# Kernel optimization log

Hardware: AMD Instinct MI355X
Metric: run time of the kernel (lower is better)

## Reference

```python
import jax, jax.numpy as jnp
import numpy as np

B, S, H = 1, 1024, 1024
E = 1024          # expert_dim
NEXP = 16         # num_experts
TOPK = 2
ALPHA = 1.702
LIMIT = 7.0


def setup_inputs() -> dict:
    key = jax.random.key(0)
    ks = jax.random.split(key, 8)
    hidden_states = jax.random.normal(ks[0], (B, S, H), dtype=jnp.float32)
    # router (gate): Linear(H, NEXP) with bias
    Wg = jax.random.normal(ks[1], (NEXP, H), dtype=jnp.float32) / np.sqrt(H)
    bg = jax.random.normal(ks[2], (NEXP,), dtype=jnp.float32) * 0.01
    # per-expert gate_up_proj: Linear(H, 2E) -> store as [NEXP, H, 2E]
    Wgu = jax.random.normal(ks[3], (NEXP, H, 2 * E), dtype=jnp.float32) / np.sqrt(H)
    bgu = jax.random.normal(ks[4], (NEXP, 2 * E), dtype=jnp.float32) * 0.01
    # per-expert down_proj: Linear(E, H) -> store as [NEXP, E, H]
    Wd = jax.random.normal(ks[5], (NEXP, E, H), dtype=jnp.float32) / np.sqrt(E)
    bd = jax.random.normal(ks[6], (NEXP, H), dtype=jnp.float32) * 0.01
    return {"hidden_states": hidden_states, "Wg": Wg, "bg": bg,
            "Wgu": Wgu, "bgu": bgu, "Wd": Wd, "bd": bd}


def _moe_forward(x, Wg, bg, Wgu, bgu, Wd, bd):
    b, s, h = x.shape
    xt = x.reshape(-1, h)                                   # [T, H]
    # router
    logits = xt @ Wg.T + bg                                 # [T, NEXP]
    # gpt_oss routing: topk over raw logits, softmax over selected
    top_vals, top_idx = jax.lax.top_k(logits, TOPK)         # [T, K]
    rw = jax.nn.softmax(top_vals.astype(jnp.float32), axis=-1).astype(xt.dtype)
    # combine weight per (token, expert): zero for unselected experts
    onehot = jax.nn.one_hot(top_idx, NEXP, dtype=xt.dtype)  # [T, K, NEXP]
    cw = jnp.einsum("tk,tke->te", rw, onehot)               # [T, NEXP]
    # dense expert compute (reference math identical to gather/scatter version)
    gu = jnp.einsum("th,ehf->tef", xt, Wgu) + bgu[None]     # [T, NEXP, 2E]
    gate = gu[..., ::2]
    up = gu[..., 1::2]
    gate = jnp.minimum(gate, LIMIT)
    up = jnp.clip(up, -LIMIT, LIMIT)
    glu = gate * jax.nn.sigmoid(gate * ALPHA)
    gated = (up + 1.0) * glu                                # [T, NEXP, E]
    out_e = jnp.einsum("tef,efh->teh", gated, Wd) + bd[None]  # [T, NEXP, H]
    out = jnp.einsum("teh,te->th", out_e, cw)               # [T, H]
    return out.reshape(b, s, h)


def reference(hidden_states, Wg, bg, Wgu, bgu, Wd, bd):
    return _moe_forward(hidden_states, Wg, bg, Wgu, bgu, Wd, bd)
```

## Files before the change

kernel.cpp:

```cpp
#include <hip/hip_runtime.h>
#include <hip/hip_bf16.h>

#define NT 1024
#define HD 1024
#define ED 1024
#define F2D 2048
#define NEXPERT 16
#define GROWS 2304
#define ALPHA_C 1.702f
#define LIMIT_C 7.0f

typedef float f32x4 __attribute__((ext_vector_type(4)));
typedef float fv4 __attribute__((ext_vector_type(4)));
typedef short short8 __attribute__((ext_vector_type(8)));
typedef unsigned int u32x4 __attribute__((ext_vector_type(4)));

__device__ __forceinline__ unsigned short f2bf(float x) {
  union { float f; unsigned int u; } v; v.f = x;
  unsigned int r = v.u + 0x7FFFu + ((v.u >> 16) & 1u);
  return (unsigned short)(r >> 16);
}
__device__ __forceinline__ unsigned int pk2(float lo, float hi) {
  return (unsigned int)f2bf(lo) | ((unsigned int)f2bf(hi) << 16);
}
__device__ __forceinline__ fv4 ldnt4(const float* p) {
  return __builtin_nontemporal_load((const fv4*)p);
}
__device__ __forceinline__ void async16(const void* g, void* l) {
  __builtin_amdgcn_global_load_lds((const __attribute__((address_space(1))) void*)g,
                                   (__attribute__((address_space(3))) void*)l, 16, 0, 0);
}

__global__ __launch_bounds__(64) void k_router(const float* __restrict__ x,
                                               const float* __restrict__ Wg,
                                               const float* __restrict__ bg,
                                               const float* __restrict__ bd,
                                               int* __restrict__ e01,
                                               float* __restrict__ w0f,
                                               float* __restrict__ w1f,
                                               unsigned short* __restrict__ Xbf,
                                               float* __restrict__ out) {
  const int t = blockIdx.x;
  const int l = threadIdx.x;
  const float4* x4 = (const float4*)(x + (size_t)t * HD);
  for (int i = 0; i < 4; ++i) {
    const int idx = l + 64 * i;
    float4 v = x4[idx];
    unsigned int a = pk2(v.x, v.y);
    unsigned int b = pk2(v.z, v.w);
    unsigned int* dst = (unsigned int*)(Xbf + (size_t)t * HD + idx * 4);
    dst[0] = a; dst[1] = b;
  }
  const int e = l & 15, qq = l >> 4;
  const float4* wg4 = (const float4*)(Wg + (size_t)e * HD);
  float s0a = 0.f, s1a = 0.f;
#pragma unroll 8
  for (int j = 0; j < 32; ++j) {
    const int i0 = qq + 8 * j;
    const int i1 = i0 + 4;
    float4 a0 = x4[i0], b0 = wg4[i0];
    float4 a1 = x4[i1], b1 = wg4[i1];
    s0a += a0.x * b0.x + a0.y * b0.y + a0.z * b0.z + a0.w * b0.w;
    s1a += a1.x * b1.x + a1.y * b1.y + a1.z * b1.z + a1.w * b1.w;
  }
  float s = s0a + s1a;
  s += __shfl_xor(s, 16);
  s += __shfl_xor(s, 32);
  const float logit = s + bg[e];
  float v0 = -1e30f, v1 = -1e30f; int i0 = 0, i1 = 0;
  for (int k = 0; k < 16; ++k) {
    float lv = __shfl(logit, k);
    if (lv > v0) { v1 = v0; i1 = i0; v0 = lv; i0 = k; }
    else if (lv > v1) { v1 = lv; i1 = k; }
  }
  const float w0 = 1.f / (1.f + __expf(v1 - v0));
  const float w1 = 1.f - w0;
  if (l == 0) {
    e01[t] = i0 | (i1 << 8);
    w0f[t] = w0;
    w1f[t] = w1;
  }
  const float4* bd0 = (const float4*)(bd + (size_t)i0 * HD);
  const float4* bd1 = (const float4*)(bd + (size_t)i1 * HD);
  float4* o4 = (float4*)(out + (size_t)t * HD);
  for (int i = 0; i < 4; ++i) {
    const int idx = l + 64 * i;
    float4 a = bd0[idx], b = bd1[idx];
    float4 r;
    r.x = w0 * a.x + w1 * b.x;
    r.y = w0 * a.y + w1 * b.y;
    r.z = w0 * a.z + w1 * b.z;
    r.w = w0 * a.w + w1 * b.w;
    o4[idx] = r;
  }
}

__global__ __launch_bounds__(1024) void k_scan(const int* __restrict__ e01,
                                               const float* __restrict__ w0f,
                                               const float* __restrict__ w1f,
                                               int* __restrict__ cnt,
                                               int* __restrict__ off,
                                               int* __restrict__ gtok,
                                               float* __restrict__ gwt) {
  __shared__ int scnt[NEXPERT];
  __shared__ int soff[NEXPERT];
  __shared__ int scur[NEXPERT];
  const int t = threadIdx.x;
  if (t < NEXPERT) { scnt[t] = 0; scur[t] = 0; }
  __syncthreads();
  const int p = e01[t];
  const int e0 = p & 255, e1 = p >> 8;
  atomicAdd(&scnt[e0], 1);
  atomicAdd(&scnt[e1], 1);
  __syncthreads();
  if (t == 0) {
    int a = 0;
    for (int e = 0; e < NEXPERT; ++e) { soff[e] = a; off[e] = a; cnt[e] = scnt[e]; a += scnt[e]; }
  }
  __syncthreads();
  int s0 = atomicAdd(&scur[e0], 1);
  gtok[soff[e0] + s0] = t; gwt[soff[e0] + s0] = w0f[t];
  int s1 = atomicAdd(&scur[e1], 1);
  gtok[soff[e1] + s1] = t; gwt[soff[e1] + s1] = w1f[t];
}

#define BSTG1 132
__global__ __launch_bounds__(512, 1) void k_gemm1(const unsigned short* __restrict__ Xbf,
                                                  const float* __restrict__ Wgu,
                                                  const float* __restrict__ bgu,
                                                  const int* __restrict__ cnt,
                                                  const int* __restrict__ off,
                                                  const int* __restrict__ gtok,
                                                  unsigned short* __restrict__ Gact) {
  const int e = blockIdx.z;
  const int Ne = cnt[e];
  const int mtile = blockIdx.y;
  if (mtile * 256 >= Ne) return;
  const int ntile = blockIdx.x;
  const int tid = threadIdx.x;
  const int lane = tid & 63;
  const int wv = tid >> 6;
  const int wm = wv >> 1;
  const int wn = wv & 1;
  const int q = lane >> 4;
  const int fr = lane & 15;
  const int base = off[e] + mtile * 256;

  __shared__ unsigned short Alds[2][256 * 32];
  __shared__ unsigned int Blds[2][16 * BSTG1];

  const int ar0 = wv * 32 + (lane >> 2);
  const int ar1 = ar0 + 16;
  const int ags0 = base + (((mtile * 256 + ar0) < Ne) ? ar0 : 0);
  const int ags1 = base + (((mtile * 256 + ar1) < Ne) ? ar1 : 0);
  const unsigned short* agp0 = Xbf + (size_t)gtok[ags0] * HD + (lane & 3) * 8;
  const unsigned short* agp1 = Xbf + (size_t)gtok[ags1] * HD + (lane & 3) * 8;
  const int aofs = wv * 1024;

  const int p2 = tid >> 5;
  const int bc = tid & 31;
  const float* Wb = Wgu + (size_t)e * HD * F2D + (size_t)(2 * p2) * F2D + ntile * 128 + bc * 4;

  f32x4 acc[4][4] = {};
  fv4 b0, b1;

  b0 = ldnt4(Wb);
  b1 = ldnt4(Wb + F2D);
  async16(agp0, Alds[0] + aofs);
  async16(agp1, Alds[0] + aofs + 512);
  {
    u32x4 pkv;
    pkv[0] = pk2(b0[0], b1[0]); pkv[1] = pk2(b0[1], b1[1]);
    pkv[2] = pk2(b0[2], b1[2]); pkv[3] = pk2(b0[3], b1[3]);
    *(u32x4*)(Blds[0] + p2 * BSTG1 + bc * 4) = pkv;
  }
  __syncthreads();

  for (int ks = 0; ks < 32; ++ks) {
    const int cur = ks & 1, nxt = cur ^ 1;
    const bool more = (ks + 1) < 32;
    if (more) {
      const float* bp = Wb + (size_t)(ks + 1) * 32 * F2D;
      b0 = ldnt4(bp);
      b1 = ldnt4(bp + F2D);
      async16(agp0 + (ks + 1) * 32, Alds[nxt] + aofs);
      async16(agp1 + (ks + 1) * 32, Alds[nxt] + aofs + 512);
    }
    short8 af[4], bfr[4];
#pragma unroll
    for (int mi = 0; mi < 4; ++mi)
      af[mi] = *(const short8*)(Alds[cur] + (wm * 64 + mi * 16 + fr) * 32 + q * 8);
#pragma unroll
    for (int ni = 0; ni < 4; ++ni) {
      const unsigned int* p = Blds[cur] + (q * 4) * BSTG1 + wn * 64 + ni * 16 + fr;
      union { unsigned int u[4]; short8 s; } uu;
      uu.u[0] = p[0]; uu.u[1] = p[BSTG1]; uu.u[2] = p[2 * BSTG1]; uu.u[3] = p[3 * BSTG1];
      bfr[ni] = uu.s;
    }
#pragma unroll
    for (int mi = 0; mi < 4; ++mi)
#pragma unroll
      for (int ni = 0; ni < 4; ++ni)
        acc[mi][ni] = __builtin_amdgcn_mfma_f32_16x16x32_bf16(af[mi], bfr[ni], acc[mi][ni], 0, 0, 0);
    if (more) {
      u32x4 pkv;
      pkv[0] = pk2(b0[0], b1[0]); pkv[1] = pk2(b0[1], b1[1]);
      pkv[2] = pk2(b0[2], b1[2]); pkv[3] = pk2(b0[3], b1[3]);
      *(u32x4*)(Blds[nxt] + p2 * BSTG1 + bc * 4) = pkv;
    }
    __syncthreads();
  }

  const float* bguE = bgu + (size_t)e * F2D + ntile * 128;
#pragma unroll
  for (int mi = 0; mi < 4; ++mi) {
#pragma unroll
    for (int ni = 0; ni < 4; ++ni) {
      const int coll = wn * 64 + ni * 16 + fr;
      const float bias = bguE[coll];
#pragma unroll
      for (int r = 0; r < 4; ++r) {
        const int srow = wm * 64 + mi * 16 + q * 4 + r;
        float v = acc[mi][ni][r] + bias;
        float pv = __shfl_xor(v, 1);
        float gate = (lane & 1) ? pv : v;
        float up   = (lane & 1) ? v : pv;
        gate = fminf(gate, LIMIT_C);
        up = fminf(fmaxf(up, -LIMIT_C), LIMIT_C);
        float glu = gate / (1.f + __expf(-ALPHA_C * gate));
        float val = (up + 1.f) * glu;
        if (!(lane & 1) && (mtile * 256 + srow) < Ne)
          Gact[(size_t)(base + srow) * ED + ((ntile * 128 + coll) >> 1)] = f2bf(val);
      }
    }
  }
}

#define BSTG2 68
__global__ __launch_bounds__(512, 2) void k_gemm2(const unsigned short* __restrict__ Gact,
                                                  const float* __restrict__ Wd,
                                                  const int* __restrict__ cnt,
                                                  const int* __restrict__ off,
                                                  const int* __restrict__ gtok,
                                                  const float* __restrict__ gwt,
                                                  float* __restrict__ out) {
  const int e = blockIdx.z;
  const int Ne = cnt[e];
  const int mtile = blockIdx.y;
  if (mtile * 256 >= Ne) return;
  const int ntile = blockIdx.x;
  const int tid = threadIdx.x;
  const int lane = tid & 63;
  const int wv = tid >> 6;
  const int q = lane >> 4;
  const int fr = lane & 15;
  const int base = off[e] + mtile * 256;

  __shared__ unsigned short Alds[2][256 * 32];
  __shared__ unsigned int Blds[2][16 * BSTG2];

  const int ar0 = wv * 32 + (lane >> 2);
  const unsigned short* agp0 = Gact + (size_t)(base + ar0) * ED + (lane & 3) * 8;
  const unsigned short* agp1 = agp0 + (size_t)16 * ED;
  const int aofs = wv * 1024;

  const int p2 = tid >> 4;
  const int bc = tid & 15;
  const float* Wb = Wd + (size_t)e * ED * HD + (size_t)(2 * p2) * HD + ntile * 64 + bc * 4;

  f32x4 acc[2][4] = {};
  fv4 b0, b1;

  if (tid < 256) {
    b0 = ldnt4(Wb);
    b1 = ldnt4(Wb + HD);
  }
  async16(agp0, Alds[0] + aofs);
  async16(agp1, Alds[0] + aofs + 512);
  if (tid < 256) {
    u32x4 pkv;
    pkv[0] = pk2(b0[0], b1[0]); pkv[1] = pk2(b0[1], b1[1]);
    pkv[2] = pk2(b0[2], b1[2]); pkv[3] = pk2(b0[3], b1[3]);
    *(u32x4*)(Blds[0] + p2 * BSTG2 + bc * 4) = pkv;
  }
  __syncthreads();

  for (int ks = 0; ks < 32; ++ks) {
    const int cur = ks & 1, nxt = cur ^ 1;
    const bool more = (ks + 1) < 32;
    if (more) {
      if (tid < 256) {
        const float* bp = Wb + (size_t)(ks + 1) * 32 * HD;
        b0 = ldnt4(bp);
        b1 = ldnt4(bp + HD);
      }
      async16(agp0 + (ks + 1) * 32, Alds[nxt] + aofs);
      async16(agp1 + (ks + 1) * 32, Alds[nxt] + aofs + 512);
    }
    short8 af[2], bfr[4];
#pragma unroll
    for (int mi = 0; mi < 2; ++mi)
      af[mi] = *(const short8*)(Alds[cur] + (wv * 32 + mi * 16 + fr) * 32 + q * 8);
#pragma unroll
    for (int ni = 0; ni < 4; ++ni) {
      const unsigned int* p = Blds[cur] + (q * 4) * BSTG2 + ni * 16 + fr;
      union { unsigned int u[4]; short8 s; } uu;
      uu.u[0] = p[0]; uu.u[1] = p[BSTG2]; uu.u[2] = p[2 * BSTG2]; uu.u[3] = p[3 * BSTG2];
      bfr[ni] = uu.s;
    }
#pragma unroll
    for (int mi = 0; mi < 2; ++mi)
#pragma unroll
      for (int ni = 0; ni < 4; ++ni)
        acc[mi][ni] = __builtin_amdgcn_mfma_f32_16x16x32_bf16(af[mi], bfr[ni], acc[mi][ni], 0, 0, 0);
    if (more && tid < 256) {
      u32x4 pkv;
      pkv[0] = pk2(b0[0], b1[0]); pkv[1] = pk2(b0[1], b1[1]);
      pkv[2] = pk2(b0[2], b1[2]); pkv[3] = pk2(b0[3], b1[3]);
      *(u32x4*)(Blds[nxt] + p2 * BSTG2 + bc * 4) = pkv;
    }
    __syncthreads();
  }

#pragma unroll
  for (int mi = 0; mi < 2; ++mi) {
#pragma unroll
    for (int r = 0; r < 4; ++r) {
      const int srow = wv * 32 + mi * 16 + q * 4 + r;
      if ((mtile * 256 + srow) < Ne) {
        const int gsl = base + srow;
        const int tok = gtok[gsl];
        const float wt = gwt[gsl];
        float* op = out + (size_t)tok * HD + ntile * 64;
#pragma unroll
        for (int ni = 0; ni < 4; ++ni) {
          const int col = ni * 16 + fr;
          atomicAdd(op + col, wt * acc[mi][ni][r]);
        }
      }
    }
  }
}

extern "C" void kernel_launch(void* const* d_in, const int* in_sizes, int n_in,
                              void* d_out, int out_size, void* d_ws, size_t ws_size,
                              hipStream_t stream) {
  const float* x   = (const float*)d_in[0];
  const float* Wg  = (const float*)d_in[1];
  const float* bg  = (const float*)d_in[2];
  const float* Wgu = (const float*)d_in[3];
  const float* bgu = (const float*)d_in[4];
  const float* Wd  = (const float*)d_in[5];
  const float* bd  = (const float*)d_in[6];
  float* out = (float*)d_out;

  int* cnt = (int*)d_ws;
  int* off = cnt + 16;
  int* e01 = off + 16;
  float* w0f = (float*)(e01 + NT);
  float* w1f = w0f + NT;
  int* gtok = (int*)(w1f + NT);
  float* gwt = (float*)(gtok + GROWS);
  unsigned short* Xbf = (unsigned short*)(gwt + GROWS);
  unsigned short* Gact = Xbf + (size_t)NT * HD;

  k_router<<<NT, 64, 0, stream>>>(x, Wg, bg, bd, e01, w0f, w1f, Xbf, out);
  k_scan<<<1, NT, 0, stream>>>(e01, w0f, w1f, cnt, off, gtok, gwt);
  k_gemm1<<<dim3(16, 2, NEXPERT), 512, 0, stream>>>(Xbf, Wgu, bgu, cnt, off, gtok, Gact);
  k_gemm2<<<dim3(16, 2, NEXPERT), 512, 0, stream>>>(Gact, Wd, cnt, off, gtok, gwt, out);
}
```

Measured before the change: 332.4 us.

## Transpose down-proj B tile in LDS via DPP and widen router blocks

The down-projection kernel now uses DPP lane swaps across groups of four lanes to transpose the packed bf16 weight pairs before storing them. Each MFMA B fragment can then be read from LDS with a single 16-byte load instead of four strided 32-bit loads. Separately, the router kernel runs with 256 threads per token, splitting the dot products across four waves and reducing the partial sums through shared memory. The cost is extra select and DPP instructions in the B staging path, plus a block barrier in the router.

```diff
diff --git a/kernel.cpp b/kernel.cpp
--- a/kernel.cpp
+++ b/kernel.cpp
@@ -31,68 +31,61 @@
                                    (__attribute__((address_space(3))) void*)l, 16, 0, 0);
 }
 
-__global__ __launch_bounds__(64) void k_router(const float* __restrict__ x,
-                                               const float* __restrict__ Wg,
-                                               const float* __restrict__ bg,
-                                               const float* __restrict__ bd,
-                                               int* __restrict__ e01,
-                                               float* __restrict__ w0f,
-                                               float* __restrict__ w1f,
-                                               unsigned short* __restrict__ Xbf,
-                                               float* __restrict__ out) {
+__global__ __launch_bounds__(256) void k_router(const float* __restrict__ x,
+                                                const float* __restrict__ Wg,
+                                                const float* __restrict__ bg,
+                                                const float* __restrict__ bd,
+                                                int* __restrict__ e01,
+                                                float* __restrict__ w0f,
+                                                float* __restrict__ w1f,
+                                                unsigned short* __restrict__ Xbf,
+                                                float* __restrict__ out) {
   const int t = blockIdx.x;
-  const int l = threadIdx.x;
+  const int tid = threadIdx.x;
+  const int w = tid >> 6;
+  const int l = tid & 63;
   const float4* x4 = (const float4*)(x + (size_t)t * HD);
-  for (int i = 0; i < 4; ++i) {
-    const int idx = l + 64 * i;
-    float4 v = x4[idx];
-    unsigned int a = pk2(v.x, v.y);
-    unsigned int b = pk2(v.z, v.w);
-    unsigned int* dst = (unsigned int*)(Xbf + (size_t)t * HD + idx * 4);
-    dst[0] = a; dst[1] = b;
+  {
+    float4 v = x4[tid];
+    unsigned int* dst = (unsigned int*)(Xbf + (size_t)t * HD + tid * 4);
+    dst[0] = pk2(v.x, v.y); dst[1] = pk2(v.z, v.w);
   }
   const int e = l & 15, qq = l >> 4;
   const float4* wg4 = (const float4*)(Wg + (size_t)e * HD);
-  float s0a = 0.f, s1a = 0.f;
-#pragma unroll 8
-  for (int j = 0; j < 32; ++j) {
-    const int i0 = qq + 8 * j;
-    const int i1 = i0 + 4;
-    float4 a0 = x4[i0], b0 = wg4[i0];
-    float4 a1 = x4[i1], b1 = wg4[i1];
-    s0a += a0.x * b0.x + a0.y * b0.y + a0.z * b0.z + a0.w * b0.w;
-    s1a += a1.x * b1.x + a1.y * b1.y + a1.z * b1.z + a1.w * b1.w;
-  }
-  float s = s0a + s1a;
+  float s = 0.f;
+#pragma unroll 4
+  for (int j = 0; j < 16; ++j) {
+    const int idx = w * 64 + qq + 4 * j;
+    float4 a = x4[idx], b = wg4[idx];
+    s += a.x * b.x + a.y * b.y + a.z * b.z + a.w * b.w;
+  }
   s += __shfl_xor(s, 16);
   s += __shfl_xor(s, 32);
-  const float logit = s + bg[e];
+  __shared__ float slog[4][16];
+  if (l < 16) slog[w][e] = s;
+  __syncthreads();
   float v0 = -1e30f, v1 = -1e30f; int i0 = 0, i1 = 0;
-  for (int k = 0; k < 16; ++k) {
-    float lv = __shfl(logit, k);
-    if (lv > v0) { v1 = v0; i1 = i0; v0 = lv; i0 = k; }
-    else if (lv > v1) { v1 = lv; i1 = k; }
+  for (int k2 = 0; k2 < 16; ++k2) {
+    float lv = slog[0][k2] + slog[1][k2] + slog[2][k2] + slog[3][k2] + bg[k2];
+    if (lv > v0) { v1 = v0; i1 = i0; v0 = lv; i0 = k2; }
+    else if (lv > v1) { v1 = lv; i1 = k2; }
   }
   const float w0 = 1.f / (1.f + __expf(v1 - v0));
   const float w1 = 1.f - w0;
-  if (l == 0) {
+  if (tid == 0) {
     e01[t] = i0 | (i1 << 8);
     w0f[t] = w0;
     w1f[t] = w1;
   }
   const float4* bd0 = (const float4*)(bd + (size_t)i0 * HD);
   const float4* bd1 = (const float4*)(bd + (size_t)i1 * HD);
-  float4* o4 = (float4*)(out + (size_t)t * HD);
-  for (int i = 0; i < 4; ++i) {
-    const int idx = l + 64 * i;
-    float4 a = bd0[idx], b = bd1[idx];
-    float4 r;
-    r.x = w0 * a.x + w1 * b.x;
-    r.y = w0 * a.y + w1 * b.y;
-    r.z = w0 * a.z + w1 * b.z;
-    r.w = w0 * a.w + w1 * b.w;
-    o4[idx] = r;
-  }
+  float4 a = bd0[tid], b = bd1[tid];
+  float4 r;
+  r.x = w0 * a.x + w1 * b.x;
+  r.y = w0 * a.y + w1 * b.y;
+  r.z = w0 * a.z + w1 * b.z;
+  r.w = w0 * a.w + w1 * b.w;
+  ((float4*)(out + (size_t)t * HD))[tid] = r;
 }
 
 __global__ __launch_bounds__(1024) void k_scan(const int* __restrict__ e01,
@@ -236,7 +229,7 @@
   }
 }
 
-#define BSTG2 68
+#define BSTG2T 20
 __global__ __launch_bounds__(512, 2) void k_gemm2(const unsigned short* __restrict__ Gact,
                                                   const float* __restrict__ Wd,
                                                   const int* __restrict__ cnt,
@@ -257,19 +250,40 @@
   const int base = off[e] + mtile * 256;
 
   __shared__ unsigned short Alds[2][256 * 32];
-  __shared__ unsigned int Blds[2][16 * BSTG2];
+  __shared__ unsigned int Blds[2][64 * BSTG2T];
 
   const int ar0 = wv * 32 + (lane >> 2);
   const unsigned short* agp0 = Gact + (size_t)(base + ar0) * ED + (lane & 3) * 8;
   const unsigned short* agp1 = agp0 + (size_t)16 * ED;
   const int aofs = wv * 1024;
 
-  const int p2 = tid >> 4;
-  const int bc = tid & 15;
-  const float* Wb = Wd + (size_t)e * ED * HD + (size_t)(2 * p2) * HD + ntile * 64 + bc * 4;
+  const int sub = lane & 3;
+  const float* Wb = Wd + (size_t)e * ED * HD + (size_t)(2 * (wv * 4 + sub)) * HD + ntile * 64 + (lane >> 2) * 4;
 
   f32x4 acc[2][4] = {};
   fv4 b0, b1;
+
+#define B2_TRANSPOSE_STORE(BUF)                                                         \
+  {                                                                                     \
+    unsigned int w0p = pk2(b0[0], b1[0]);                                               \
+    unsigned int w1p = pk2(b0[1], b1[1]);                                               \
+    unsigned int w2p = pk2(b0[2], b1[2]);                                               \
+    unsigned int w3p = pk2(b0[3], b1[3]);                                               \
+    unsigned int X0 = sub == 0 ? w0p : sub == 1 ? w1p : sub == 2 ? w2p : w3p;           \
+    unsigned int X1 = sub == 0 ? w1p : sub == 1 ? w0p : sub == 2 ? w3p : w2p;           \
+    unsigned int X2 = sub == 0 ? w2p : sub == 1 ? w3p : sub == 2 ? w0p : w1p;           \
+    unsigned int X3 = sub == 0 ? w3p : sub == 1 ? w2p : sub == 2 ? w1p : w0p;           \
+    unsigned int r0 = X0;                                                               \
+    unsigned int r1 = (unsigned int)__builtin_amdgcn_update_dpp((int)X1, (int)X1, 0xB1, 0xF, 0xF, 0); \
+    unsigned int r2 = (unsigned int)__builtin_amdgcn_update_dpp((int)X2, (int)X2, 0x4E, 0xF, 0xF, 0); \
+    unsigned int r3 = (unsigned int)__builtin_amdgcn_update_dpp((int)X3, (int)X3, 0x1B, 0xF, 0xF, 0); \
+    u32x4 tt;                                                                           \
+    tt[0] = sub == 0 ? r0 : sub == 1 ? r1 : sub == 2 ? r2 : r3;                         \
+    tt[1] = sub == 0 ? r1 : sub == 1 ? r0 : sub == 2 ? r3 : r2;                         \
+    tt[2] = sub == 0 ? r2 : sub == 1 ? r3 : sub == 2 ? r0 : r1;                         \
+    tt[3] = sub == 0 ? r3 : sub == 1 ? r2 : sub == 2 ? r1 : r0;                         \
+    *(u32x4*)(Blds[BUF] + lane * BSTG2T + wv * 4) = tt;                                 \
+  }
 
   if (tid < 256) {
     b0 = ldnt4(Wb);
@@ -277,12 +291,7 @@
   }
   async16(agp0, Alds[0] + aofs);
   async16(agp1, Alds[0] + aofs + 512);
-  if (tid < 256) {
-    u32x4 pkv;
-    pkv[0] = pk2(b0[0], b1[0]); pkv[1] = pk2(b0[1], b1[1]);
-    pkv[2] = pk2(b0[2], b1[2]); pkv[3] = pk2(b0[3], b1[3]);
-    *(u32x4*)(Blds[0] + p2 * BSTG2 + bc * 4) = pkv;
-  }
+  if (tid < 256) B2_TRANSPOSE_STORE(0)
   __syncthreads();
 
   for (int ks = 0; ks < 32; ++ks) {
@@ -302,23 +311,14 @@
     for (int mi = 0; mi < 2; ++mi)
       af[mi] = *(const short8*)(Alds[cur] + (wv * 32 + mi * 16 + fr) * 32 + q * 8);
 #pragma unroll
-    for (int ni = 0; ni < 4; ++ni) {
-      const unsigned int* p = Blds[cur] + (q * 4) * BSTG2 + ni * 16 + fr;
-      union { unsigned int u[4]; short8 s; } uu;
-      uu.u[0] = p[0]; uu.u[1] = p[BSTG2]; uu.u[2] = p[2 * BSTG2]; uu.u[3] = p[3 * BSTG2];
-      bfr[ni] = uu.s;
-    }
+    for (int ni = 0; ni < 4; ++ni)
+      bfr[ni] = *(const short8*)(Blds[cur] + (ni * 16 + fr) * BSTG2T + q * 4);
 #pragma unroll
     for (int mi = 0; mi < 2; ++mi)
 #pragma unroll
       for (int ni = 0; ni < 4; ++ni)
         acc[mi][ni] = __builtin_amdgcn_mfma_f32_16x16x32_bf16(af[mi], bfr[ni], acc[mi][ni], 0, 0, 0);
-    if (more && tid < 256) {
-      u32x4 pkv;
-      pkv[0] = pk2(b0[0], b1[0]); pkv[1] = pk2(b0[1], b1[1]);
-      pkv[2] = pk2(b0[2], b1[2]); pkv[3] = pk2(b0[3], b1[3]);
-      *(u32x4*)(Blds[nxt] + p2 * BSTG2 + bc * 4) = pkv;
-    }
+    if (more && tid < 256) B2_TRANSPOSE_STORE(nxt)
     __syncthreads();
   }
 
@@ -364,7 +364,7 @@
   unsigned short* Xbf = (unsigned short*)(gwt + GROWS);
   unsigned short* Gact = Xbf + (size_t)NT * HD;
 
-  k_router<<<NT, 64, 0, stream>>>(x, Wg, bg, bd, e01, w0f, w1f, Xbf, out);
+  k_router<<<NT, 256, 0, stream>>>(x, Wg, bg, bd, e01, w0f, w1f, Xbf, out);
   k_scan<<<1, NT, 0, stream>>>(e01, w0f, w1f, cnt, off, gtok, gwt);
   k_gemm1<<<dim3(16, 2, NEXPERT), 512, 0, stream>>>(Xbf, Wgu, bgu, cnt, off, gtok, Gact);
   k_gemm2<<<dim3(16, 2, NEXPERT), 512, 0, stream>>>(Gact, Wd, cnt, off, gtok, gwt, out);
```

Result: no change. 330.8 us (-0.5%).
